# Optimization experiments

Hardware: AMD Instinct MI355X
Metric: run time of the kernel (lower is better)

Reference implementation:

```python
import jax, jax.numpy as jnp
import numpy as np

IN_CH = 16
OUT_CH = 64
G = 4
K = 3
EXP_CH = G * IN_CH * OUT_CH  # 4096 expanded channels
SET_LEN = G * IN_CH          # 64 indices per pooling set
B, H, W = 8, 56, 56


def setup_inputs() -> dict:
    key = jax.random.key(0)
    k1, k2, k3, k4 = jax.random.split(key, 4)
    x = jax.random.normal(k1, (B, IN_CH, H, W), dtype=jnp.float32)
    # grouped conv weight: [out_channels=EXP_CH, in_ch/groups=1, K, K]
    weight = jax.random.normal(k2, (EXP_CH, 1, K, K), dtype=jnp.float32) * 0.1
    bias = jax.random.normal(k3, (EXP_CH,), dtype=jnp.float32) * 0.1
    # channel_idx_sets: OUT_CH sets, each SET_LEN indices into the EXP_CH channels
    idx_sets = jax.random.randint(k4, (OUT_CH, SET_LEN), 0, EXP_CH, dtype=jnp.int32)
    return {"x": x, "weight": weight, "bias": bias, "idx_sets": idx_sets}


def reference(x, weight, bias, idx_sets):
    # Grouped conv2d: groups = IN_CH, output channels = G*IN_CH*OUT_CH
    out = jax.lax.conv_general_dilated(
        x, weight,
        window_strides=(1, 1),
        padding=((1, 1), (1, 1)),
        feature_group_count=IN_CH,
        dimension_numbers=("NCHW", "OIHW", "NCHW"),
    )
    out = out + bias[None, :, None, None]  # [B, EXP_CH, H, W]
    # FusedMultiPool: for each output channel j, max over channels idx_sets[j]
    gathered = out[:, idx_sets]            # [B, OUT_CH, SET_LEN, H, W]
    return jnp.max(gathered, axis=2)       # [B, OUT_CH, H, W]
```

## Files before the change

### kernel.cpp

```cpp
#include <hip/hip_runtime.h>

#define IN_CH    16
#define OUT_CH   64
#define SET_LEN  64
#define BB       8
#define HH       56
#define WW       56

#define TILEROWS 8
#define NTILES   7
#define LDSROWS  (TILEROWS + 2)
#define LROW     56
#define LDS_XN   (IN_CH * LDSROWS * LROW)
#define NVEC     (IN_CH * LDSROWS * 14)

typedef float f32x2 __attribute__((ext_vector_type(2)));
typedef float f32x4 __attribute__((ext_vector_type(4)));

static __device__ __forceinline__ f32x2 splat2(float s) { return (f32x2){s, s}; }

__global__ __launch_bounds__(256, 2)
void rptn_fused_kernel(const float* __restrict__ x,
                       const float* __restrict__ w,
                       const float* __restrict__ bias,
                       const int*   __restrict__ idx,
                       float*       __restrict__ out) {
    const int oc   = blockIdx.x;
    const int tile = blockIdx.y;
    const int b    = blockIdx.z;
    const int tid  = threadIdx.x;
    const int tx   = tid & 63;
    const int grp  = __builtin_amdgcn_readfirstlane(tid >> 6);

    __shared__ float s_x[LDS_XN];
    __shared__ f32x4 s_w[SET_LEN * 3];
    __shared__ int   s_cnt[IN_CH];
    __shared__ int   s_pos[IN_CH];
    __shared__ int   s_eord[SET_LEN];

    if (tid < IN_CH) s_cnt[tid] = 0;
    __syncthreads();
    int my_e = 0;
    if (tid < SET_LEN) {
        my_e = idx[oc * SET_LEN + tid];
        atomicAdd(&s_cnt[my_e >> 8], 1);
    }
    __syncthreads();
    if (tid == 0) {
        int run = 0;
        for (int c = 0; c < IN_CH; ++c) { s_pos[c] = run; run += s_cnt[c]; }
    }
    __syncthreads();
    if (tid < SET_LEN) {
        int p = atomicAdd(&s_pos[my_e >> 8], 1);
        s_eord[p] = my_e;
    }
    __syncthreads();

    float* s_wf = (float*)s_w;
    for (int i = tid; i < SET_LEN * 12; i += 256) {
        const int j    = i / 12;
        const int comp = i - j * 12;
        const int e    = s_eord[j];
        float v;
        if (comp < 9)        v = w[e * 9 + comp];
        else if (comp == 9)  v = bias[e];
        else if (comp == 10) v = __int_as_float(e >> 8);
        else                 v = 0.0f;
        s_wf[j * 12 + comp] = v;
    }

    const int r0 = tile * TILEROWS;
    const float* xb = x + (size_t)b * IN_CH * HH * WW;
    #pragma unroll
    for (int it = 0; it < 9; ++it) {
        const int v = tid + it * 256;
        if (it < 8 || v < NVEC) {
            const int c   = v / (LDSROWS * 14);
            const int rem = v - c * (LDSROWS * 14);
            const int r   = rem / 14;
            const int q   = rem - r * 14;
            const int gr  = r0 - 1 + r;
            f32x4 val = {0, 0, 0, 0};
            if ((unsigned)gr < (unsigned)HH)
                val = *(const f32x4*)(xb + (c * HH + gr) * WW + q * 4);
            *(f32x4*)&s_x[(c * LDSROWS + r) * LROW + q * 4] = val;
        }
    }
    __syncthreads();

    const bool  lanev = (tx < WW);
    const int   txr   = lanev ? tx : 0;
    const int   txl   = (txr > 0)  ? txr - 1 : 0;
    const int   txp   = (txr < 55) ? txr + 1 : 55;
    const float lm    = (txr == 0)  ? 0.0f : 1.0f;
    const float rm    = (txr == 55) ? 0.0f : 1.0f;

    f32x2 acc = { -__builtin_inff(), -__builtin_inff() };
    int ccur = -1;
    f32x2 v00={0,0},v01={0,0},v02={0,0};
    f32x2 v10={0,0},v11={0,0},v12={0,0};
    f32x2 v20={0,0},v21={0,0},v22={0,0};

    #pragma unroll 2
    for (int k = 0; k < SET_LEN; ++k) {
        const f32x4 q0 = s_w[k * 3 + 0];
        const f32x4 q1 = s_w[k * 3 + 1];
        const f32x4 q2 = s_w[k * 3 + 2];
        const int c = __float_as_int(q2.z);
        if (c != ccur) {
            ccur = c;
            const float* sp = &s_x[(c * LDSROWS + grp * 2) * LROW];
            const float n00=sp[txl]*lm,        n01=sp[txr],        n02=sp[txp]*rm;
            const float n10=sp[LROW+txl]*lm,   n11=sp[LROW+txr],   n12=sp[LROW+txp]*rm;
            const float n20=sp[2*LROW+txl]*lm, n21=sp[2*LROW+txr], n22=sp[2*LROW+txp]*rm;
            const float n30=sp[3*LROW+txl]*lm, n31=sp[3*LROW+txr], n32=sp[3*LROW+txp]*rm;
            v00=(f32x2){n00,n10}; v01=(f32x2){n01,n11}; v02=(f32x2){n02,n12};
            v10=(f32x2){n10,n20}; v11=(f32x2){n11,n21}; v12=(f32x2){n12,n22};
            v20=(f32x2){n20,n30}; v21=(f32x2){n21,n31}; v22=(f32x2){n22,n32};
        }
        f32x2 t0 = __builtin_elementwise_fma(splat2(q0.z), v02,
                   __builtin_elementwise_fma(splat2(q0.y), v01,
                   __builtin_elementwise_fma(splat2(q0.x), v00, splat2(q2.y))));
        f32x2 t1 = __builtin_elementwise_fma(splat2(q1.y), v12,
                   __builtin_elementwise_fma(splat2(q1.x), v11,
                                             splat2(q0.w) * v10));
        f32x2 t2 = __builtin_elementwise_fma(splat2(q2.x), v22,
                   __builtin_elementwise_fma(splat2(q1.w), v21,
                                             splat2(q1.z) * v20));
        const f32x2 s = t0 + (t1 + t2);
        acc.x = fmaxf(acc.x, s.x);
        acc.y = fmaxf(acc.y, s.y);
    }

    if (lanev) {
        const size_t o = (((size_t)b * OUT_CH + oc) * HH + (r0 + grp * 2)) * WW + tx;
        out[o]      = acc.x;
        out[o + WW] = acc.y;
    }
}

extern "C" void kernel_launch(void* const* d_in, const int* in_sizes, int n_in,
                              void* d_out, int out_size, void* d_ws, size_t ws_size,
                              hipStream_t stream) {
    const float* x    = (const float*)d_in[0];
    const float* w    = (const float*)d_in[1];
    const float* bias = (const float*)d_in[2];
    const int*   idx  = (const int*)d_in[3];
    float*       out  = (float*)d_out;

    dim3 grid(OUT_CH, NTILES, BB);
    dim3 block(256);
    rptn_fused_kernel<<<grid, block, 0, stream>>>(x, w, bias, idx, out);
}
```

Baseline: 122.8 us.

## Hoist per-channel weight sort and gather into a separate presort kernel

Adds a small presort kernel that, for each output channel, sorts its index set by input channel and writes packed weights, bias and channel id to workspace once. The main kernel then drops its per-block atomics, barriers and scattered weight gathers, reading the packed weights straight from global memory (uniform, likely scalar or cached loads) instead of from LDS, and unrolls the loop further. This adds a second kernel launch and a global-memory dependency in place of the redundant per-tile setup. A fallback path keeps the old kernel when the workspace is too small.

```diff
diff --git a/kernel.cpp b/kernel.cpp
--- a/kernel.cpp
+++ b/kernel.cpp
@@ -14,17 +14,136 @@
 #define LDS_XN   (IN_CH * LDSROWS * LROW)
 #define NVEC     (IN_CH * LDSROWS * 14)
 
+#define WS_NEEDED (OUT_CH * SET_LEN * 12 * 4)
+
 typedef float f32x2 __attribute__((ext_vector_type(2)));
 typedef float f32x4 __attribute__((ext_vector_type(4)));
 
 static __device__ __forceinline__ f32x2 splat2(float s) { return (f32x2){s, s}; }
 
+__global__ __launch_bounds__(64)
+void rptn_presort(const float* __restrict__ w, const float* __restrict__ bias,
+                  const int* __restrict__ idx, float* __restrict__ ws_w) {
+    const int oc = blockIdx.x;
+    const int t  = threadIdx.x;
+    __shared__ int cnt[IN_CH], pos[IN_CH], eord[SET_LEN];
+
+    if (t < IN_CH) cnt[t] = 0;
+    __syncthreads();
+    const int e = idx[oc * SET_LEN + t];
+    const int c = e >> 8;
+    atomicAdd(&cnt[c], 1);
+    __syncthreads();
+    if (t == 0) {
+        int run = 0;
+        for (int i = 0; i < IN_CH; ++i) { pos[i] = run; run += cnt[i]; }
+    }
+    __syncthreads();
+    const int p = atomicAdd(&pos[c], 1);
+    eord[p] = e;
+    __syncthreads();
+
+    const int    es  = eord[t];
+    float*       dst = ws_w + ((size_t)oc * SET_LEN + t) * 12;
+    const float* src = w + es * 9;
+    #pragma unroll
+    for (int i = 0; i < 9; ++i) dst[i] = src[i];
+    dst[9]  = bias[es];
+    dst[10] = __int_as_float(es >> 8);
+    dst[11] = 0.0f;
+}
+
 __global__ __launch_bounds__(256, 2)
 void rptn_fused_kernel(const float* __restrict__ x,
-                       const float* __restrict__ w,
-                       const float* __restrict__ bias,
-                       const int*   __restrict__ idx,
+                       const float* __restrict__ ws_w,
                        float*       __restrict__ out) {
+    const int oc   = blockIdx.x;
+    const int tile = blockIdx.y;
+    const int b    = blockIdx.z;
+    const int tid  = threadIdx.x;
+    const int tx   = tid & 63;
+    const int grp  = __builtin_amdgcn_readfirstlane(tid >> 6);
+
+    __shared__ float s_x[LDS_XN];
+
+    const int r0 = tile * TILEROWS;
+    const float* xb = x + (size_t)b * IN_CH * HH * WW;
+    #pragma unroll
+    for (int it = 0; it < 9; ++it) {
+        const int v = tid + it * 256;
+        if (it < 8 || v < NVEC) {
+            const int c   = v / (LDSROWS * 14);
+            const int rem = v - c * (LDSROWS * 14);
+            const int r   = rem / 14;
+            const int q   = rem - r * 14;
+            const int gr  = r0 - 1 + r;
+            f32x4 val = {0, 0, 0, 0};
+            if ((unsigned)gr < (unsigned)HH)
+                val = *(const f32x4*)(xb + (c * HH + gr) * WW + q * 4);
+            *(f32x4*)&s_x[(c * LDSROWS + r) * LROW + q * 4] = val;
+        }
+    }
+    __syncthreads();
+
+    const bool  lanev = (tx < WW);
+    const int   txr   = lanev ? tx : 0;
+    const int   txl   = (txr > 0)  ? txr - 1 : 0;
+    const int   txp   = (txr < 55) ? txr + 1 : 55;
+    const float lm    = (txr == 0)  ? 0.0f : 1.0f;
+    const float rm    = (txr == 55) ? 0.0f : 1.0f;
+
+    f32x2 acc = { -__builtin_inff(), -__builtin_inff() };
+    int ccur = -1;
+    f32x2 v00={0,0},v01={0,0},v02={0,0};
+    f32x2 v10={0,0},v11={0,0},v12={0,0};
+    f32x2 v20={0,0},v21={0,0},v22={0,0};
+
+    const f32x4* wt = (const f32x4*)ws_w + (size_t)oc * SET_LEN * 3;
+
+    #pragma unroll 4
+    for (int k = 0; k < SET_LEN; ++k) {
+        const f32x4 q0 = wt[k * 3 + 0];
+        const f32x4 q1 = wt[k * 3 + 1];
+        const f32x4 q2 = wt[k * 3 + 2];
+        const int c = __float_as_int(q2.z);
+        if (c != ccur) {
+            ccur = c;
+            const float* sp = &s_x[(c * LDSROWS + grp * 2) * LROW];
+            const float n00=sp[txl]*lm,        n01=sp[txr],        n02=sp[txp]*rm;
+            const float n10=sp[LROW+txl]*lm,   n11=sp[LROW+txr],   n12=sp[LROW+txp]*rm;
+            const float n20=sp[2*LROW+txl]*lm, n21=sp[2*LROW+txr], n22=sp[2*LROW+txp]*rm;
+            const float n30=sp[3*LROW+txl]*lm, n31=sp[3*LROW+txr], n32=sp[3*LROW+txp]*rm;
+            v00=(f32x2){n00,n10}; v01=(f32x2){n01,n11}; v02=(f32x2){n02,n12};
+            v10=(f32x2){n10,n20}; v11=(f32x2){n11,n21}; v12=(f32x2){n12,n22};
+            v20=(f32x2){n20,n30}; v21=(f32x2){n21,n31}; v22=(f32x2){n22,n32};
+        }
+        f32x2 t0 = __builtin_elementwise_fma(splat2(q0.z), v02,
+                   __builtin_elementwise_fma(splat2(q0.y), v01,
+                   __builtin_elementwise_fma(splat2(q0.x), v00, splat2(q2.y))));
+        f32x2 t1 = __builtin_elementwise_fma(splat2(q1.y), v12,
+                   __builtin_elementwise_fma(splat2(q1.x), v11,
+                                             splat2(q0.w) * v10));
+        f32x2 t2 = __builtin_elementwise_fma(splat2(q2.x), v22,
+                   __builtin_elementwise_fma(splat2(q1.w), v21,
+                                             splat2(q1.z) * v20));
+        const f32x2 s = t0 + (t1 + t2);
+        acc.x = fmaxf(acc.x, s.x);
+        acc.y = fmaxf(acc.y, s.y);
+    }
+
+    if (lanev) {
+        const size_t o = (((size_t)b * OUT_CH + oc) * HH + (r0 + grp * 2)) * WW + tx;
+        out[o]      = acc.x;
+        out[o + WW] = acc.y;
+    }
+}
+
+__global__ __launch_bounds__(256, 2)
+void rptn_fused_fallback(const float* __restrict__ x,
+                         const float* __restrict__ w,
+                         const float* __restrict__ bias,
+                         const int*   __restrict__ idx,
+                         float*       __restrict__ out) {
     const int oc   = blockIdx.x;
     const int tile = blockIdx.y;
     const int b    = blockIdx.z;
@@ -151,5 +270,12 @@
 
     dim3 grid(OUT_CH, NTILES, BB);
     dim3 block(256);
-    rptn_fused_kernel<<<grid, block, 0, stream>>>(x, w, bias, idx, out);
-}
+
+    if (ws_size >= (size_t)WS_NEEDED) {
+        float* ws_w = (float*)d_ws;
+        rptn_presort<<<dim3(OUT_CH), dim3(64), 0, stream>>>(w, bias, idx, ws_w);
+        rptn_fused_kernel<<<grid, block, 0, stream>>>(x, ws_w, out);
+    } else {
+        rptn_fused_fallback<<<grid, block, 0, stream>>>(x, w, bias, idx, out);
+    }
+}
```

Measured after the change: 122.8 us. Within noise of the previous version (+0.0%).
